# Kernel optimization log

Measured on AMD Instinct MI355X. Metric: run time of the kernel, lower is better.

Reference implementation:

```python
import jax, jax.numpy as jnp
import numpy as np

B, N, C = 32, 2048, 3
K = 20
E = 64  # embed_dim
BN_EPS = 1e-5


def setup_inputs() -> dict:
    key = jax.random.key(0)
    k1, k2, k3, k4 = jax.random.split(key, 4)
    xyz = jax.random.normal(k1, (B, N, C), dtype=jnp.float32)
    # Conv2d(6, E, kernel_size=1, bias=False) -> weight [E, 6]
    W = jax.random.normal(k2, (E, 2 * C), dtype=jnp.float32) * (1.0 / np.sqrt(2 * C))
    gamma = jnp.ones((E,), dtype=jnp.float32)
    beta = jnp.zeros((E,), dtype=jnp.float32)
    return {"xyz": xyz, "W": W, "gamma": gamma, "beta": beta}


def _forward(xyz, W, gamma, beta):
    # --- KNN: idx of k largest of negative squared distance ---
    dot = jnp.einsum("bnc,bmc->bnm", xyz, xyz)            # [B,N,N]
    xx = jnp.sum(xyz * xyz, axis=-1)                       # [B,N]
    pdist = 2.0 * dot - xx[:, :, None] - xx[:, None, :]    # -||xi-xj||^2
    idx = jax.lax.top_k(pdist, K)[1]                        # [B,N,K] int32
    # --- gather neighbors (index_points) ---
    grouped = jax.vmap(lambda pts, i: pts[i])(xyz, idx)    # [B,N,K,C]
    xyz_rep = jnp.broadcast_to(xyz[:, :, None, :], (B, N, K, C))
    edge = jnp.concatenate([xyz_rep, grouped - xyz_rep], axis=-1)  # [B,N,K,2C]
    # --- 1x1 conv (pointwise matmul) ---
    h = jnp.einsum("bnkc,ec->bnke", edge, W)               # [B,N,K,E]
    # --- BatchNorm2d (training-mode batch stats over B,N,K per channel) ---
    mean = jnp.mean(h, axis=(0, 1, 2))
    var = jnp.mean(jnp.square(h - mean), axis=(0, 1, 2))   # biased var
    hn = (h - mean) * jax.lax.rsqrt(var + BN_EPS) * gamma + beta
    # --- hardswish: x * relu6(x + 3) / 6 ---
    a = hn * jnp.clip(hn + 3.0, 0.0, 6.0) * (1.0 / 6.0)
    # --- max over k neighbors, output [B,E,N] ---
    x = jnp.max(a, axis=2)                                  # [B,N,E]
    return xyz, jnp.transpose(x, (0, 2, 1))                 # [B,E,N]


def reference(xyz, W, gamma, beta):
    return _forward(xyz, W, gamma, beta)
```

## Files before the change

kernel.cpp:

```cpp
#include <hip/hip_runtime.h>
#include <math.h>

#define Bdim 32
#define Ndim 2048
#define Cdim 3
#define Kdim 20
#define Edim 64
#define NPART 27
#define NBLK1 2048
#define CNT (Bdim * Ndim * Kdim)

#define NEG_INF __int_as_float(0xFF800000)

#define DPPU(v, ctrl) \
  ((unsigned)__builtin_amdgcn_update_dpp((int)(v), (int)(v), (ctrl), 0xf, 0xf, false))
#define DPPF(v, ctrl) \
  (__int_as_float(__builtin_amdgcn_update_dpp(__float_as_int(v), __float_as_int(v), (ctrl), 0xf, 0xf, false)))

__device__ __forceinline__ unsigned red_max_u32_l63(unsigned v) {
  unsigned t;
  t = DPPU(v, 0x121); v = (v > t) ? v : t;
  t = DPPU(v, 0x122); v = (v > t) ? v : t;
  t = DPPU(v, 0x124); v = (v > t) ? v : t;
  t = DPPU(v, 0x128); v = (v > t) ? v : t;
  t = DPPU(v, 0x142); v = (v > t) ? v : t;
  t = DPPU(v, 0x143); v = (v > t) ? v : t;
  return v;
}

__device__ __forceinline__ float red_max_f32_l63(float v) {
  float t;
  t = DPPF(v, 0x121); v = fmaxf(v, t);
  t = DPPF(v, 0x122); v = fmaxf(v, t);
  t = DPPF(v, 0x124); v = fmaxf(v, t);
  t = DPPF(v, 0x128); v = fmaxf(v, t);
  t = DPPF(v, 0x142); v = fmaxf(v, t);
  t = DPPF(v, 0x143); v = fmaxf(v, t);
  return v;
}

__device__ __forceinline__ float red_add_f32_l63(float v) {
  float t;
  t = DPPF(v, 0x121); v += t;
  t = DPPF(v, 0x122); v += t;
  t = DPPF(v, 0x124); v += t;
  t = DPPF(v, 0x128); v += t;
  t = DPPF(v, 0x142); v += t;
  t = DPPF(v, 0x143); v += t;
  return v;
}

__device__ __forceinline__ float sreadf(float v, int l) {
  return __int_as_float(__builtin_amdgcn_readlane(__float_as_int(v), l));
}

__global__ __launch_bounds__(512) void k1_knn_stats(
    const float* __restrict__ xyz, int* __restrict__ idx_out,
    float* __restrict__ partials) {
  __shared__ float4 pts[Ndim];
  __shared__ float red[8][NPART];

  const int b = blockIdx.y;
  const int tid = threadIdx.x;
  const float* xb = xyz + (size_t)b * Ndim * Cdim;

  float* sp = (float*)&pts[0];
  for (int g = tid; g < Ndim * Cdim; g += 512) {
    sp[(g / 3) * 4 + (g % 3)] = xb[g];
  }
  __syncthreads();
  for (int p = tid; p < Ndim; p += 512) {
    float4 q = pts[p];
    pts[p].w = q.x * q.x + q.y * q.y + q.z * q.z;
  }
  __syncthreads();

  const int w = tid >> 6;
  const int lane = tid & 63;
  const unsigned il = 2047u - (unsigned)lane;

  float acc[NPART];
#pragma unroll
  for (int c = 0; c < NPART; ++c) acc[c] = 0.0f;

  for (int s = 0; s < 4; ++s) {
    const int i = blockIdx.x * 32 + w * 4 + s;
    const float4 pi = pts[i];

    unsigned mask = 0u;
    float h1 = NEG_INF, h2 = NEG_INF, h3 = NEG_INF;
    unsigned l1 = 0u, l2 = 0u, l3 = 0u;

#pragma unroll 8
    for (int t = 0; t < 32; ++t) {
      const int j = t * 64 + lane;
      const float4 pj = pts[j];
      const float dot = pi.x * pj.x + pi.y * pj.y + pi.z * pj.z;
      const float pd = 2.0f * dot - pi.w - pj.w;
      const unsigned tl = il - (unsigned)(t * 64);
      const bool b1 = pd > h1;
      const bool b2 = pd > h2;
      const bool b3 = pd > h3;
      h3 = b3 ? (b2 ? h2 : pd) : h3;  l3 = b3 ? (b2 ? l2 : tl) : l3;
      h2 = b2 ? (b1 ? h1 : pd) : h2;  l2 = b2 ? (b1 ? l1 : tl) : l2;
      h1 = b1 ? pd : h1;              l1 = b1 ? tl : l1;
    }

    unsigned myJ = 0u;
    for (int r = 0; r < Kdim; ++r) {
      const float bm = red_max_f32_l63(h1);
      const float bestk = sreadf(bm, 63);

      const unsigned long long mb = __ballot(h1 == bestk);
      unsigned jwin;
      if ((mb & (mb - 1ull)) == 0ull) {
        const int wl = __ffsll((unsigned long long)mb) - 1;
        jwin = 2047u - (unsigned)__builtin_amdgcn_readlane((int)l1, wl);
      } else {
        unsigned cand = (h1 == bestk) ? l1 : 0u;
        cand = red_max_u32_l63(cand);
        jwin = 2047u - (unsigned)__builtin_amdgcn_readlane((int)cand, 63);
      }
      if (lane == r) myJ = jwin;

      if ((unsigned)lane == (jwin & 63u)) {
        mask |= (1u << (jwin >> 6));
        if (h2 != NEG_INF) {
          h1 = h2; l1 = l2; h2 = h3; l2 = l3; h3 = NEG_INF;
        } else {
          float a1 = NEG_INF, a2 = NEG_INF, a3 = NEG_INF;
          unsigned c1 = 0u, c2 = 0u, c3 = 0u;
          for (int t = 0; t < 32; ++t) {
            if (mask & (1u << t)) continue;
            const int j = t * 64 + lane;
            const float4 pj = pts[j];
            const float dot = pi.x * pj.x + pi.y * pj.y + pi.z * pj.z;
            const float pd = 2.0f * dot - pi.w - pj.w;
            const unsigned tl = il - (unsigned)(t * 64);
            const bool b1 = pd > a1;
            const bool b2 = pd > a2;
            const bool b3 = pd > a3;
            a3 = b3 ? (b2 ? a2 : pd) : a3;  c3 = b3 ? (b2 ? c2 : tl) : c3;
            a2 = b2 ? (b1 ? a1 : pd) : a2;  c2 = b2 ? (b1 ? c1 : tl) : c2;
            a1 = b1 ? pd : a1;              c1 = b1 ? tl : c1;
          }
          h1 = a1; l1 = c1; h2 = a2; l2 = c2; h3 = a3; l3 = c3;
        }
      }
    }

    if (lane < Kdim) {
      idx_out[((size_t)b * Ndim + i) * Kdim + lane] = (int)myJ;
      const float4 pj = pts[myJ];
      float ev[6];
      ev[0] = pi.x; ev[1] = pi.y; ev[2] = pi.z;
      ev[3] = pj.x - pi.x; ev[4] = pj.y - pi.y; ev[5] = pj.z - pi.z;
#pragma unroll
      for (int a = 0; a < 6; ++a) acc[a] += ev[a];
      int c = 6;
#pragma unroll
      for (int a = 0; a < 6; ++a)
#pragma unroll
        for (int d = a; d < 6; ++d) { acc[c] += ev[a] * ev[d]; ++c; }
    }
  }

#pragma unroll
  for (int c = 0; c < NPART; ++c) {
    const float v = red_add_f32_l63(acc[c]);
    if (lane == 63) red[w][c] = v;
  }
  __syncthreads();
  if (tid < NPART) {
    const int bid = blockIdx.y * gridDim.x + blockIdx.x;
    float v = 0.0f;
#pragma unroll
    for (int q = 0; q < 8; ++q) v += red[q][tid];
    partials[(size_t)bid * NPART + tid] = v;
  }
}

__global__ __launch_bounds__(256) void k2_bnstats(
    const float* __restrict__ partials, const float* __restrict__ W,
    const float* __restrict__ gamma, const float* __restrict__ beta,
    float* __restrict__ ss) {
  __shared__ double stat[NPART];
  __shared__ double red[4];
  const int tid = threadIdx.x;
  const int lane = tid & 63;
  const int w = tid >> 6;

  for (int c = 0; c < NPART; ++c) {
    double v = 0.0;
    for (int p = tid; p < NBLK1; p += 256) v += (double)partials[(size_t)p * NPART + c];
#pragma unroll
    for (int d = 1; d < 64; d <<= 1) v += __shfl_xor(v, d, 64);
    if (lane == 0) red[w] = v;
    __syncthreads();
    if (tid == 0) stat[c] = red[0] + red[1] + red[2] + red[3];
    __syncthreads();
  }

  if (tid < Edim) {
    const double inv = 1.0 / (double)CNT;
    double mu[6];
#pragma unroll
    for (int c = 0; c < 6; ++c) mu[c] = stat[c] * inv;
    double wv[6];
#pragma unroll
    for (int c = 0; c < 6; ++c) wv[c] = (double)W[tid * 6 + c];
    double m = 0.0;
#pragma unroll
    for (int c = 0; c < 6; ++c) m += wv[c] * mu[c];
    double q = 0.0;
    int s = 6;
#pragma unroll
    for (int a = 0; a < 6; ++a)
#pragma unroll
      for (int d = a; d < 6; ++d) {
        q += (a == d ? 1.0 : 2.0) * wv[a] * wv[d] * (stat[s] * inv);
        ++s;
      }
    const double var = q - m * m;
    const double rstd = 1.0 / sqrt(var + 1e-5);
    const float scale = (float)((double)gamma[tid] * rstd);
    const float shift = (float)((double)beta[tid] - m * rstd * (double)gamma[tid]);
    ss[tid] = scale;
    ss[Edim + tid] = shift;
  }
}

__global__ __launch_bounds__(512) void k3_out(
    const float* __restrict__ xyz, const int* __restrict__ idx,
    const float* __restrict__ W, const float* __restrict__ ss,
    float* __restrict__ out) {
  __shared__ float4 pts[Ndim];
  __shared__ float sm[128][65];
  const int b = blockIdx.y;
  const int n0 = blockIdx.x * 128;
  const int tid = threadIdx.x;
  const int w = tid >> 6;
  const int lane = tid & 63;
  const float* xb = xyz + (size_t)b * Ndim * Cdim;

  float* sp = (float*)&pts[0];
  for (int g = tid; g < Ndim * Cdim; g += 512) {
    sp[(g / 3) * 4 + (g % 3)] = xb[g];
  }
  __syncthreads();

  float wv[6];
#pragma unroll
  for (int c = 0; c < 6; ++c) wv[c] = W[lane * 6 + c];
  const float scale = ss[lane];
  const float shift = ss[Edim + lane];

  for (int s = 0; s < 16; ++s) {
    const int i = n0 + w * 16 + s;
    const float4 pi = pts[i];
    const float hbase = wv[0] * pi.x + wv[1] * pi.y + wv[2] * pi.z;
    const int* ip = idx + ((size_t)b * Ndim + i) * Kdim;
    float m = -INFINITY;
    for (int k = 0; k < Kdim; ++k) {
      const int j = ip[k];
      const float4 pj = pts[j];
      const float h = hbase + wv[3] * (pj.x - pi.x) + wv[4] * (pj.y - pi.y) +
                      wv[5] * (pj.z - pi.z);
      const float a = h * scale + shift;
      const float r6 = fminf(fmaxf(a + 3.0f, 0.0f), 6.0f);
      const float hs = a * r6 * (1.0f / 6.0f);
      m = fmaxf(m, hs);
    }
    sm[w * 16 + s][lane] = m;
  }
  __syncthreads();

#pragma unroll
  for (int r = 0; r < 8; ++r) {
    const int e = r * 8 + w;
    out[((size_t)b * Edim + e) * Ndim + n0 + lane] = sm[lane][e];
    out[((size_t)b * Edim + e) * Ndim + n0 + 64 + lane] = sm[64 + lane][e];
  }
}

extern "C" void kernel_launch(void* const* d_in, const int* in_sizes, int n_in,
                              void* d_out, int out_size, void* d_ws, size_t ws_size,
                              hipStream_t stream) {
  const float* xyz = (const float*)d_in[0];
  const float* W = (const float*)d_in[1];
  const float* gamma = (const float*)d_in[2];
  const float* beta = (const float*)d_in[3];
  float* out = (float*)d_out;

  char* ws = (char*)d_ws;
  int* idx = (int*)ws;
  float* partials = (float*)(ws + (size_t)Bdim * Ndim * Kdim * 4);
  float* ss = (float*)(ws + (size_t)Bdim * Ndim * Kdim * 4 + (size_t)NBLK1 * NPART * 4);

  hipMemcpyAsync(out, xyz, (size_t)Bdim * Ndim * Cdim * sizeof(float),
                 hipMemcpyDeviceToDevice, stream);

  k1_knn_stats<<<dim3(Ndim / 32, Bdim), 512, 0, stream>>>(xyz, idx, partials);
  k2_bnstats<<<1, 256, 0, stream>>>(partials, W, gamma, beta, ss);
  k3_out<<<dim3(Ndim / 128, Bdim), 512, 0, stream>>>(
      xyz, idx, W, ss, out + (size_t)Bdim * Ndim * Cdim);
}
```

Measured before the change: 250.5 us.

## Process four query points per wave jointly in KNN scan and selection

The KNN kernel now handles the four query points of each wave together. Each loaded candidate point is reused across four distance/top-3 updates, which cuts LDS loads and adds independent work for latency hiding. The 20-round selection loop interleaves the four queries, stores tile indices instead of reversed global indices, and turns the pop branch into selects. The conv kernel also makes the neighbor index wave-uniform with readfirstlane, so the point fetch becomes a broadcast. The cost is higher register pressure from the four sets of top-3 state.

Result: slower. 354.8 us (+41.7%).

```diff
diff --git a/kernel.cpp b/kernel.cpp
--- a/kernel.cpp
+++ b/kernel.cpp
@@ -77,84 +77,102 @@
 
   const int w = tid >> 6;
   const int lane = tid & 63;
-  const unsigned il = 2047u - (unsigned)lane;
 
   float acc[NPART];
 #pragma unroll
   for (int c = 0; c < NPART; ++c) acc[c] = 0.0f;
 
-  for (int s = 0; s < 4; ++s) {
-    const int i = blockIdx.x * 32 + w * 4 + s;
-    const float4 pi = pts[i];
-
-    unsigned mask = 0u;
-    float h1 = NEG_INF, h2 = NEG_INF, h3 = NEG_INF;
-    unsigned l1 = 0u, l2 = 0u, l3 = 0u;
-
-#pragma unroll 8
-    for (int t = 0; t < 32; ++t) {
-      const int j = t * 64 + lane;
-      const float4 pj = pts[j];
-      const float dot = pi.x * pj.x + pi.y * pj.y + pi.z * pj.z;
-      const float pd = 2.0f * dot - pi.w - pj.w;
-      const unsigned tl = il - (unsigned)(t * 64);
-      const bool b1 = pd > h1;
-      const bool b2 = pd > h2;
-      const bool b3 = pd > h3;
-      h3 = b3 ? (b2 ? h2 : pd) : h3;  l3 = b3 ? (b2 ? l2 : tl) : l3;
-      h2 = b2 ? (b1 ? h1 : pd) : h2;  l2 = b2 ? (b1 ? l1 : tl) : l2;
-      h1 = b1 ? pd : h1;              l1 = b1 ? tl : l1;
+  const int i0 = blockIdx.x * 32 + w * 4;
+
+  float4 pi[4];
+#pragma unroll
+  for (int p = 0; p < 4; ++p) pi[p] = pts[i0 + p];
+
+  float h1[4], h2[4], h3[4];
+  unsigned l1[4], l2[4], l3[4], mask[4];
+#pragma unroll
+  for (int p = 0; p < 4; ++p) {
+    h1[p] = h2[p] = h3[p] = NEG_INF;
+    l1[p] = l2[p] = l3[p] = 0u;
+    mask[p] = 0u;
+  }
+
+#pragma unroll 4
+  for (int t = 0; t < 32; ++t) {
+    const float4 pj = pts[t * 64 + lane];
+#pragma unroll
+    for (int p = 0; p < 4; ++p) {
+      const float dot = pi[p].x * pj.x + pi[p].y * pj.y + pi[p].z * pj.z;
+      const float pd = 2.0f * dot - pi[p].w - pj.w;
+      const bool b1 = pd > h1[p];
+      const bool b2 = pd > h2[p];
+      const bool b3 = pd > h3[p];
+      h3[p] = b3 ? (b2 ? h2[p] : pd) : h3[p];
+      l3[p] = b3 ? (b2 ? l2[p] : (unsigned)t) : l3[p];
+      h2[p] = b2 ? (b1 ? h1[p] : pd) : h2[p];
+      l2[p] = b2 ? (b1 ? l1[p] : (unsigned)t) : l2[p];
+      h1[p] = b1 ? pd : h1[p];
+      l1[p] = b1 ? (unsigned)t : l1[p];
     }
-
-    unsigned myJ = 0u;
-    for (int r = 0; r < Kdim; ++r) {
-      const float bm = red_max_f32_l63(h1);
+  }
+
+  unsigned myJ[4] = {0u, 0u, 0u, 0u};
+  for (int r = 0; r < Kdim; ++r) {
+#pragma unroll
+    for (int p = 0; p < 4; ++p) {
+      const float bm = red_max_f32_l63(h1[p]);
       const float bestk = sreadf(bm, 63);
 
-      const unsigned long long mb = __ballot(h1 == bestk);
+      const unsigned long long mb = __ballot(h1[p] == bestk);
       unsigned jwin;
       if ((mb & (mb - 1ull)) == 0ull) {
         const int wl = __ffsll((unsigned long long)mb) - 1;
-        jwin = 2047u - (unsigned)__builtin_amdgcn_readlane((int)l1, wl);
+        jwin = ((unsigned)__builtin_amdgcn_readlane((int)l1[p], wl)) * 64u +
+               (unsigned)wl;
       } else {
-        unsigned cand = (h1 == bestk) ? l1 : 0u;
+        unsigned cand =
+            (h1[p] == bestk) ? (2047u - (l1[p] * 64u + (unsigned)lane)) : 0u;
         cand = red_max_u32_l63(cand);
         jwin = 2047u - (unsigned)__builtin_amdgcn_readlane((int)cand, 63);
       }
-      if (lane == r) myJ = jwin;
-
-      if ((unsigned)lane == (jwin & 63u)) {
-        mask |= (1u << (jwin >> 6));
-        if (h2 != NEG_INF) {
-          h1 = h2; l1 = l2; h2 = h3; l2 = l3; h3 = NEG_INF;
-        } else {
-          float a1 = NEG_INF, a2 = NEG_INF, a3 = NEG_INF;
-          unsigned c1 = 0u, c2 = 0u, c3 = 0u;
-          for (int t = 0; t < 32; ++t) {
-            if (mask & (1u << t)) continue;
-            const int j = t * 64 + lane;
-            const float4 pj = pts[j];
-            const float dot = pi.x * pj.x + pi.y * pj.y + pi.z * pj.z;
-            const float pd = 2.0f * dot - pi.w - pj.w;
-            const unsigned tl = il - (unsigned)(t * 64);
-            const bool b1 = pd > a1;
-            const bool b2 = pd > a2;
-            const bool b3 = pd > a3;
-            a3 = b3 ? (b2 ? a2 : pd) : a3;  c3 = b3 ? (b2 ? c2 : tl) : c3;
-            a2 = b2 ? (b1 ? a1 : pd) : a2;  c2 = b2 ? (b1 ? c1 : tl) : c2;
-            a1 = b1 ? pd : a1;              c1 = b1 ? tl : c1;
-          }
-          h1 = a1; l1 = c1; h2 = a2; l2 = c2; h3 = a3; l3 = c3;
+      if (lane == r) myJ[p] = jwin;
+
+      const bool win = ((unsigned)lane == (jwin & 63u));
+      const bool pop = win && (h2[p] != NEG_INF);
+      const bool resc = win && (h2[p] == NEG_INF);
+      mask[p] |= win ? (1u << (jwin >> 6)) : 0u;
+      h1[p] = pop ? h2[p] : h1[p];  l1[p] = pop ? l2[p] : l1[p];
+      h2[p] = pop ? h3[p] : h2[p];  l2[p] = pop ? l3[p] : l2[p];
+      h3[p] = pop ? NEG_INF : h3[p];
+      if (resc) {
+        float a1 = NEG_INF, a2 = NEG_INF, a3 = NEG_INF;
+        unsigned c1 = 0u, c2 = 0u, c3 = 0u;
+        for (int t = 0; t < 32; ++t) {
+          if (mask[p] & (1u << t)) continue;
+          const int j = t * 64 + lane;
+          const float4 pj = pts[j];
+          const float dot = pi[p].x * pj.x + pi[p].y * pj.y + pi[p].z * pj.z;
+          const float pd = 2.0f * dot - pi[p].w - pj.w;
+          const bool b1 = pd > a1;
+          const bool b2 = pd > a2;
+          const bool b3 = pd > a3;
+          a3 = b3 ? (b2 ? a2 : pd) : a3;  c3 = b3 ? (b2 ? c2 : (unsigned)t) : c3;
+          a2 = b2 ? (b1 ? a1 : pd) : a2;  c2 = b2 ? (b1 ? c1 : (unsigned)t) : c2;
+          a1 = b1 ? pd : a1;              c1 = b1 ? (unsigned)t : c1;
         }
+        h1[p] = a1; l1[p] = c1; h2[p] = a2; l2[p] = c2; h3[p] = a3; l3[p] = c3;
       }
     }
-
+  }
+
+#pragma unroll
+  for (int p = 0; p < 4; ++p) {
     if (lane < Kdim) {
-      idx_out[((size_t)b * Ndim + i) * Kdim + lane] = (int)myJ;
-      const float4 pj = pts[myJ];
+      idx_out[((size_t)b * Ndim + (i0 + p)) * Kdim + lane] = (int)myJ[p];
+      const float4 pj = pts[myJ[p]];
       float ev[6];
-      ev[0] = pi.x; ev[1] = pi.y; ev[2] = pi.z;
-      ev[3] = pj.x - pi.x; ev[4] = pj.y - pi.y; ev[5] = pj.z - pi.z;
+      ev[0] = pi[p].x; ev[1] = pi[p].y; ev[2] = pi[p].z;
+      ev[3] = pj.x - pi[p].x; ev[4] = pj.y - pi[p].y; ev[5] = pj.z - pi[p].z;
 #pragma unroll
       for (int a = 0; a < 6; ++a) acc[a] += ev[a];
       int c = 6;
@@ -262,7 +280,7 @@
     const int* ip = idx + ((size_t)b * Ndim + i) * Kdim;
     float m = -INFINITY;
     for (int k = 0; k < Kdim; ++k) {
-      const int j = ip[k];
+      const int j = __builtin_amdgcn_readfirstlane(ip[k]);
       const float4 pj = pts[j];
       const float h = hbase + wv[3] * (pj.x - pi.x) + wv[4] * (pj.y - pi.y) +
                       wv[5] * (pj.z - pi.z);
```
